# Kernel optimization log

Measured on AMD Instinct MI355X. Metric: run time of the kernel, lower is better.

The kernel has to match this reference:

```python
import jax, jax.numpy as jnp
import numpy as np

T_MIN, T_MAX = 0.6, 1.6
SIM_LO, SIM_HI = 0.5, 0.9
LN_EPS = 1e-5


def _layernorm(x, gamma, beta):
    mu = jnp.mean(x, axis=-1, keepdims=True)
    var = jnp.mean((x - mu) ** 2, axis=-1, keepdims=True)
    return (x - mu) * jax.lax.rsqrt(var + LN_EPS) * gamma + beta


def _cos_sim(a, b, eps=1e-8):
    num = jnp.sum(a * b, axis=-1)
    na = jnp.maximum(jnp.sqrt(jnp.sum(a * a, axis=-1)), eps)
    nb = jnp.maximum(jnp.sqrt(jnp.sum(b * b, axis=-1)), eps)
    return num / (na * nb)


def setup_inputs() -> dict:
    key = jax.random.key(0)
    B, L, D = 2, 4096, 512
    ks = jax.random.split(key, 10)
    s = 0.02
    return {
        "x": jax.random.normal(ks[0], (B, L, D), dtype=jnp.float32),
        "Wq": jax.random.normal(ks[1], (D, D), dtype=jnp.float32) * s,
        "Wk": jax.random.normal(ks[2], (D, D), dtype=jnp.float32) * s,
        "Wv": jax.random.normal(ks[3], (D, D), dtype=jnp.float32) * s,
        "Wp": jax.random.normal(ks[4], (D, D), dtype=jnp.float32) * s,
        "W1": jax.random.normal(ks[5], (4 * D, D), dtype=jnp.float32) * s,
        "b1": jnp.zeros((4 * D,), dtype=jnp.float32),
        "W2": jax.random.normal(ks[6], (D, 4 * D), dtype=jnp.float32) * s,
        "b2": jnp.zeros((D,), dtype=jnp.float32),
        "gamma": jnp.ones((D,), dtype=jnp.float32),
        "beta": jnp.zeros((D,), dtype=jnp.float32),
    }


def reference(x, Wq, Wk, Wv, Wp, W1, b1, W2, b2, gamma, beta):
    B, L, D = x.shape
    xn = _layernorm(x, gamma, beta)
    # TinyAttn with T=1.0, causal=True (torch Linear: x @ W.T)
    Q = jnp.einsum("bld,ed->ble", xn, Wq)
    K = jnp.einsum("bld,ed->ble", xn, Wk)
    V = jnp.einsum("bld,ed->ble", xn, Wv)
    scores = jnp.einsum("bld,bmd->blm", Q, K) / jnp.sqrt(jnp.asarray(D, x.dtype))
    causal = jnp.triu(jnp.ones((L, L), dtype=bool), 1)
    scores = jnp.where(causal, jnp.asarray(-1e30, x.dtype), scores)
    attn = jax.nn.softmax(scores, axis=-1)  # [B, L, L]
    out = jnp.einsum("blm,bmd->bld", attn, V)
    out = jnp.einsum("bld,ed->ble", out, Wp)
    ctx = x + out
    h = _layernorm(ctx, gamma, beta)
    h = jax.nn.gelu(jnp.einsum("bld,fd->blf", h, W1) + b1, approximate=False)
    ctx = ctx + jnp.einsum("blf,df->bld", h, W2) + b2

    # AdaptiveController on last-token attention row
    last_attn = attn[:, -1]  # [B, L]
    p = jnp.clip(last_attn, 1e-9, None)
    H = -jnp.sum(p * jnp.log(p), axis=-1)  # [B]
    Hn = (H - H.min()) / (H.max() - H.min() + 1e-9)
    Hm = jax.lax.stop_gradient(jnp.mean(Hn))  # detached in torch
    T = T_MIN + (T_MAX - T_MIN) * Hm
    sim_th = SIM_HI - (SIM_HI - SIM_LO) * Hm

    # UnconsciousStack: single forward -> stack holds only the just-pushed (K, V), detached.
    q_vec = jnp.mean(Q[:, -1], axis=0, keepdims=True)  # [1, D]
    K_rep = jax.lax.stop_gradient(jnp.mean(K, axis=1))  # [B, D]
    s = jnp.mean(_cos_sim(q_vec, K_rep))  # scalar
    hit = s >= sim_th

    K_cat = jnp.concatenate([K, jax.lax.stop_gradient(K)], axis=1)  # [B, 2L, D]
    V_cat = jnp.concatenate([V, jax.lax.stop_gradient(V)], axis=1)
    scores2 = jnp.einsum("bld,bmd->blm", Q, K_cat) / jnp.sqrt(jnp.asarray(D, x.dtype))
    attn2 = jax.nn.softmax(scores2 / T, axis=-1)  # [B, L, 2L], no causal mask
    reatt = jnp.einsum("blm,bmd->bld", attn2, V_cat)
    ctx = ctx + jnp.where(hit, reatt, jnp.zeros_like(reatt))
    return ctx
```

## Files before the change

### kernel.cpp

```cpp
#include <hip/hip_runtime.h>
#include <math.h>

#define BATCH 2
#define SEQ 4096
#define DIM 512
#define FF 2048
#define NROWS (BATCH*SEQ)
#define KT 32
#define RSQRT_D 0.044194173824159216f

typedef __attribute__((ext_vector_type(8))) short short8;
typedef __attribute__((ext_vector_type(4))) short short4v;
typedef __attribute__((ext_vector_type(4))) float f32x4;

__device__ __forceinline__ float gelu_f(float v) {
    return 0.5f * v * (1.0f + erff(v * 0.70710678118654752440f));
}
__device__ __forceinline__ short bf16b(float x) {
    union { float f; unsigned u; } c; c.f = x;
    unsigned r = (c.u + 0x7FFFu + ((c.u >> 16) & 1u)) >> 16;
    return (short)r;
}
__device__ __forceinline__ float bf16f(short h) {
    union { unsigned u; float f; } c; c.u = ((unsigned)(unsigned short)h) << 16;
    return c.f;
}
__device__ __forceinline__ void gload16(const void* g, void* l) {
    __builtin_amdgcn_global_load_lds(
        (const __attribute__((address_space(1))) unsigned int*)g,
        (__attribute__((address_space(3))) unsigned int*)l, 16, 0, 0);
}
__device__ __forceinline__ float blk_sum256(float v, volatile float* sm) {
    #pragma unroll
    for (int o = 32; o; o >>= 1) v += __shfl_xor(v, o);
    __syncthreads();
    if ((threadIdx.x & 63) == 0) sm[threadIdx.x >> 6] = v;
    __syncthreads();
    return sm[0] + sm[1] + sm[2] + sm[3];
}

__global__ __launch_bounds__(256) void f2bf_all(
        const float* __restrict__ Wq, const float* __restrict__ Wk,
        const float* __restrict__ Wv, const float* __restrict__ Wp,
        const float* __restrict__ W1, const float* __restrict__ W2,
        short* __restrict__ Wcat, short* __restrict__ Wpb,
        short* __restrict__ W1b, short* __restrict__ W2b)
{
    int i = blockIdx.x * 256 + threadIdx.x;
    const float* src; short* dst; int loc;
    if      (i <  32768) { src = Wq; dst = Wcat;          loc = i; }
    else if (i <  65536) { src = Wk; dst = Wcat + 262144; loc = i - 32768; }
    else if (i <  98304) { src = Wv; dst = Wcat + 524288; loc = i - 65536; }
    else if (i < 131072) { src = Wp; dst = Wpb;           loc = i - 98304; }
    else if (i < 262144) { src = W1; dst = W1b;           loc = i - 131072; }
    else                 { src = W2; dst = W2b;           loc = i - 262144; }
    const float4* p = (const float4*)(src + (size_t)loc * 8);
    float4 a = p[0], b = p[1];
    short8 r;
    r[0]=bf16b(a.x); r[1]=bf16b(a.y); r[2]=bf16b(a.z); r[3]=bf16b(a.w);
    r[4]=bf16b(b.x); r[5]=bf16b(b.y); r[6]=bf16b(b.z); r[7]=bf16b(b.w);
    *(short8*)(dst + (size_t)loc * 8) = r;
}

__global__ __launch_bounds__(256) void ln_kernel(const float* __restrict__ x,
        const float* __restrict__ g, const float* __restrict__ be,
        short* __restrict__ o)
{
    int row  = blockIdx.x * 4 + (threadIdx.x >> 6);
    int lane = threadIdx.x & 63;
    const float4* xr = (const float4*)(x + (size_t)row * DIM);
    float4 v0 = xr[lane*2], v1 = xr[lane*2+1];
    float s = v0.x+v0.y+v0.z+v0.w + v1.x+v1.y+v1.z+v1.w;
    #pragma unroll
    for (int off = 32; off; off >>= 1) s += __shfl_xor(s, off);
    float mu = s * (1.0f/DIM);
    float d[8] = {v0.x-mu, v0.y-mu, v0.z-mu, v0.w-mu, v1.x-mu, v1.y-mu, v1.z-mu, v1.w-mu};
    float q = 0.f;
    #pragma unroll
    for (int j = 0; j < 8; ++j) q += d[j]*d[j];
    #pragma unroll
    for (int off = 32; off; off >>= 1) q += __shfl_xor(q, off);
    float rs = rsqrtf(q * (1.0f/DIM) + 1e-5f);
    const float4* g4 = (const float4*)g;
    const float4* b4 = (const float4*)be;
    float4 ga = g4[lane*2], gb = g4[lane*2+1];
    float4 ba = b4[lane*2], bb = b4[lane*2+1];
    float gv[8] = {ga.x,ga.y,ga.z,ga.w, gb.x,gb.y,gb.z,gb.w};
    float bv[8] = {ba.x,ba.y,ba.z,ba.w, bb.x,bb.y,bb.z,bb.w};
    short8 r;
    #pragma unroll
    for (int j = 0; j < 8; ++j) r[j] = bf16b(d[j]*rs*gv[j] + bv[j]);
    *(short8*)(o + (size_t)row * DIM + lane*8) = r;
}

template<int TM, int TAG>
__global__ __launch_bounds__(256) void gemm_v4(
        const short* __restrict__ A, const short* __restrict__ W,
        const float* __restrict__ bias, const float* __restrict__ res,
        float* __restrict__ Cf, short* __restrict__ Cb,
        short* __restrict__ CbK, short* __restrict__ CbV,
        int K, int sa, int sw, int sc, int act, int accum)
{
    constexpr int MI = TM / 32;
    constexpr int ASZ = TM * 32;
    __shared__ short As[3 * ASZ];
    __shared__ short Ws[3 * 4096];
    int tid = threadIdx.x;
    int m0 = blockIdx.y * TM, n0 = blockIdx.x * 128;
    int w = tid >> 6, lane = tid & 63;
    int wr = (w >> 1) * (TM/2), wc = (w & 1) * 64;
    int lr = lane & 15, lg = lane >> 4;
    int srow = tid >> 2, skoff = (tid & 3) * 8;
    const short* Ab = A + (size_t)(m0 + srow) * sa + skoff;
    const short* Wb = W + (size_t)(n0 + srow) * sw + skoff;

    #define STAGE_G(buf, kk) do { \
        gload16(Ab + (kk),                    As + (buf)*ASZ + tid*8); \
        if constexpr (TM == 128) \
            gload16(Ab + (size_t)64*sa + (kk), As + (buf)*ASZ + 2048 + tid*8); \
        gload16(Wb + (kk),                    Ws + (buf)*4096 + tid*8); \
        gload16(Wb + (size_t)64*sw + (kk),    Ws + (buf)*4096 + 2048 + tid*8); } while(0)

    f32x4 acc[MI][4];
    f32x4 zero = {0.f, 0.f, 0.f, 0.f};
    #pragma unroll
    for (int i = 0; i < MI; ++i)
        #pragma unroll
        for (int j = 0; j < 4; ++j) acc[i][j] = zero;

    int NKB = K >> 5;
    STAGE_G(0, 0);
    STAGE_G(1, 32);
    int cur = 0;
    for (int kb = 0; kb < NKB; ++kb) {
        __builtin_amdgcn_s_barrier();
        asm volatile("" ::: "memory");
        if (kb + 2 < NKB) {
            int nb = cur + 2; if (nb >= 3) nb -= 3;
            STAGE_G(nb, (kb + 2) * 32);
            if constexpr (TM == 128) asm volatile("s_waitcnt vmcnt(8)" ::: "memory");
            else                     asm volatile("s_waitcnt vmcnt(6)" ::: "memory");
        } else if (kb + 1 < NKB) {
            if constexpr (TM == 128) asm volatile("s_waitcnt vmcnt(4)" ::: "memory");
            else                     asm volatile("s_waitcnt vmcnt(3)" ::: "memory");
        } else {
            asm volatile("s_waitcnt vmcnt(0)" ::: "memory");
        }
        __builtin_amdgcn_s_barrier();
        asm volatile("" ::: "memory");
        short8 a[MI], b[4];
        #pragma unroll
        for (int i = 0; i < MI; ++i) a[i] = *(const short8*)(As + cur*ASZ + (wr + i*16 + lr)*32 + lg*8);
        #pragma unroll
        for (int j = 0; j < 4; ++j) b[j] = *(const short8*)(Ws + cur*4096 + (wc + j*16 + lr)*32 + lg*8);
        #pragma unroll
        for (int i = 0; i < MI; ++i)
            #pragma unroll
            for (int j = 0; j < 4; ++j)
                acc[i][j] = __builtin_amdgcn_mfma_f32_16x16x32_bf16(a[i], b[j], acc[i][j], 0, 0, 0);
        cur = (cur + 1 == 3) ? 0 : cur + 1;
    }
    #undef STAGE_G

    #pragma unroll
    for (int i = 0; i < MI; ++i) {
        #pragma unroll
        for (int r = 0; r < 4; ++r) {
            size_t m = (size_t)m0 + wr + i*16 + lg*4 + r;
            #pragma unroll
            for (int j = 0; j < 4; ++j) {
                int n = n0 + wc + j*16 + lr;
                float v = acc[i][j][r];
                if (bias) v += bias[n];
                if (act)  v = gelu_f(v);
                if (CbK) {
                    int seg = n >> 9, nl = n & 511;
                    short* dst = (seg == 0) ? Cb : (seg == 1) ? CbK : CbV;
                    dst[m * 512 + nl] = bf16b(v);
                } else {
                    if (res) v += res[m * sc + n];
                    size_t idx = m * sc + n;
                    if (Cf) { if (accum) Cf[idx] += v; else Cf[idx] = v; }
                    if (Cb) Cb[idx] = bf16b(v);
                }
            }
        }
    }
}

__global__ __launch_bounds__(256) void vtrans(const short* __restrict__ V,
                                              short* __restrict__ Vt)
{
    __shared__ short t_s[64][72];
    int l0 = blockIdx.x * 64, d0 = blockIdx.y * 64, b = blockIdx.z;
    int t = threadIdx.x;
    const short* src = V + (size_t)b * SEQ * DIM;
    #pragma unroll
    for (int it = 0; it < 2; ++it) {
        int r = (t >> 3) + it * 32, c = (t & 7) * 8;
        *(short8*)&t_s[r][c] = *(const short8*)(src + (size_t)(l0 + r) * DIM + d0 + c);
    }
    __syncthreads();
    short* dst = Vt + (size_t)b * DIM * SEQ;
    #pragma unroll
    for (int it = 0; it < 2; ++it) {
        int r = (t >> 3) + it * 32, c = (t & 7) * 8;
        short8 v;
        #pragma unroll
        for (int j = 0; j < 8; ++j) v[j] = t_s[c + j][r];
        *(short8*)(dst + (size_t)(d0 + r) * SEQ + l0 + c) = v;
    }
}

__global__ __launch_bounds__(512, 2) void attn_v8(
        const short* __restrict__ Q, const short* __restrict__ K,
        const short* __restrict__ Vt, short* __restrict__ Opart,
        float* __restrict__ Mpart, float* __restrict__ Lpart,
        float scale, const float* __restrict__ scale_ptr,
        const float* __restrict__ gate, int causal, int NC, int ncs)
{
    if (gate && gate[0] == 0.0f) return;
    if (scale_ptr) scale = scale_ptr[0];
    extern __shared__ short lds[];
    short* k_s  = lds;
    short* v_s  = lds + 32768;
    short* p_s  = lds + 65536;
    float* ss_s = (float*)(lds + 69632);

    int tid = threadIdx.x, w = tid >> 6, lane = tid & 63;
    int rg = w >> 1, dh = w & 1;
    int lr = lane & 15, lg = lane >> 4;

    int bid = blockIdx.x;
    int c  = bid & (NC - 1);
    int b  = (bid >> ncs) & 1;
    int ip = bid >> (ncs + 1);
    int jj0 = ip, jj1 = 63 - ip;
    int TA = causal ? 2*(ip+1)  : 128;
    int TB = causal ? 2*(64-ip) : 128;
    int Ttot = TA + TB;
    int s0 = (Ttot * c) >> ncs, s1 = (Ttot * (c+1)) >> ncs;

    size_t bofs = (size_t)b * SEQ * DIM;
    size_t vofs = (size_t)b * DIM * SEQ;
    f32x4 zero = {0.f, 0.f, 0.f, 0.f};

    for (int sg = 0; sg < 2; ++sg) {
        int j  = sg ? jj1 : jj0;
        int ta = sg ? (max(s0, TA) - TA) : s0;
        int tb = sg ? (s1 - TA)          : min(s1, TA);
        if (ta >= tb) continue;
        int qw0 = j*64 + rg*16;

        short8 qf[8];
        #pragma unroll
        for (int kc = 0; kc < 8; ++kc)
            qf[kc] = *(const short8*)(Q + bofs + (size_t)(qw0 + lr)*DIM
                                      + dh*256 + kc*32 + lg*8);

        f32x4 o[16];
        #pragma unroll
        for (int df = 0; df < 16; ++df) o[df] = zero;
        float mreg[4] = {-1e30f,-1e30f,-1e30f,-1e30f};
        float lreg[4] = {0.f,0.f,0.f,0.f};
        int rowg[4];
        #pragma unroll
        for (int r = 0; r < 4; ++r) rowg[r] = qw0 + lg*4 + r;

        int cur = 0;
        {
            int k0s = ta * KT;
            #pragma unroll
            for (int s4 = 0; s4 < 4; ++s4) {
                int slot = tid + s4*512;
                int row = slot >> 6, cg = slot & 63;
                gload16(K + bofs + (size_t)(k0s + row)*DIM + ((cg ^ (row & 7)) << 3),
                        k_s + slot*8);
                int dpair = slot >> 3, low = slot & 7;
                int d = dpair*2 + (low & 1);
                int kg = (low >> 1) ^ (dpair & 3);
                gload16(Vt + vofs + (size_t)d*SEQ + k0s + kg*8,
                        v_s + slot*8);
            }
        }
        __syncthreads();

        for (int t = ta; t < tb; ++t) {
            int k0 = t * KT;
            if (t + 1 < tb) {
                int k0s = (t + 1) * KT;
                int bo = (cur ^ 1) * 16384;
                #pragma unroll
                for (int s4 = 0; s4 < 4; ++s4) {
                    int slot = tid + s4*512;
                    int row = slot >> 6, cg = slot & 63;
                    gload16(K + bofs + (size_t)(k0s + row)*DIM + ((cg ^ (row & 7)) << 3),
                            k_s + bo + slot*8);
                    int dpair = slot >> 3, low = slot & 7;
                    int d = dpair*2 + (low & 1);
                    int kg = (low >> 1) ^ (dpair & 3);
                    gload16(Vt + vofs + (size_t)d*SEQ + k0s + kg*8,
                            v_s + bo + slot*8);
                }
            }
            f32x4 ss[2];
            ss[0] = zero; ss[1] = zero;
            const short* kb = k_s + cur*16384;
            #pragma unroll
            for (int kc = 0; kc < 8; ++kc) {
                #pragma unroll
                for (int kf = 0; kf < 2; ++kf) {
                    int row = kf*16 + lr;
                    int dg = dh*32 + kc*4 + lg;
                    short8 kk = *(const short8*)(kb + row*512 + ((dg ^ (row & 7)) << 3));
                    ss[kf] = __builtin_amdgcn_mfma_f32_16x16x32_bf16(qf[kc], kk, ss[kf], 0, 0, 0);
                }
            }
            *(f32x4*)(ss_s + w*512 + lane*8)     = ss[0];
            *(f32x4*)(ss_s + w*512 + lane*8 + 4) = ss[1];
            asm volatile("s_waitcnt lgkmcnt(0)" ::: "memory");
            __builtin_amdgcn_s_barrier();
            __builtin_amdgcn_sched_barrier(0);
            f32x4 po0 = *(const f32x4*)(ss_s + (w^1)*512 + lane*8);
            f32x4 po1 = *(const f32x4*)(ss_s + (w^1)*512 + lane*8 + 4);
            bool needmask = causal && (k0 + KT - 1 > qw0);
            #pragma unroll
            for (int r = 0; r < 4; ++r) {
                float s0v = (ss[0][r] + po0[r]) * scale;
                float s1v = (ss[1][r] + po1[r]) * scale;
                if (needmask) {
                    if (k0 + lr      > rowg[r]) s0v = -1e30f;
                    if (k0 + 16 + lr > rowg[r]) s1v = -1e30f;
                }
                ss[0][r] = s0v; ss[1][r] = s1v;
            }
            float pm[4];
            bool tg = false;
            #pragma unroll
            for (int r = 0; r < 4; ++r) {
                pm[r] = fmaxf(ss[0][r], ss[1][r]);
                tg |= (pm[r] > mreg[r] + 8.0f);
            }
            if (__any(tg)) {
                #pragma unroll
                for (int r = 0; r < 4; ++r) {
                    float v = pm[r];
                    v = fmaxf(v, __shfl_xor(v, 1));
                    v = fmaxf(v, __shfl_xor(v, 2));
                    v = fmaxf(v, __shfl_xor(v, 4));
                    v = fmaxf(v, __shfl_xor(v, 8));
                    float nm = fmaxf(mreg[r], v);
                    float fr = __expf(mreg[r] - nm);
                    mreg[r] = nm;
                    lreg[r] *= fr;
                    #pragma unroll
                    for (int df = 0; df < 16; ++df) o[df][r] *= fr;
                }
            }
            #pragma unroll
            for (int kf = 0; kf < 2; ++kf) {
                #pragma unroll
                for (int r = 0; r < 4; ++r) {
                    float sv = ss[kf][r];
                    float p = (sv < -1e29f) ? 0.0f : __expf(sv - mreg[r]);
                    lreg[r] += p;
                    int row = lg*4 + r;
                    int oct = kf*2 + (lr >> 3);
                    p_s[w*512 + row*32 + ((oct ^ r ^ (lg & 3)) << 3) + (lr & 7)] = bf16b(p);
                }
            }
            short8 pa = *(const short8*)(p_s + w*512 + lr*32
                         + ((lg ^ (lr & 3) ^ ((lr >> 2) & 3)) << 3));
            const short* vb = v_s + cur*16384;
            #pragma unroll
            for (int df = 0; df < 16; ++df) {
                int d = dh*256 + df*16 + lr;
                int slot16 = (d >> 1)*8 + (((lg ^ ((d >> 1) & 3)) << 1) | (d & 1));
                short8 vv = *(const short8*)(vb + slot16*8);
                o[df] = __builtin_amdgcn_mfma_f32_16x16x32_bf16(pa, vv, o[df], 0, 0, 0);
            }
            __syncthreads();
            cur ^= 1;
        }

        #pragma unroll
        for (int r = 0; r < 4; ++r) {
            float v = lreg[r];
            v += __shfl_xor(v, 1);
            v += __shfl_xor(v, 2);
            v += __shfl_xor(v, 4);
            v += __shfl_xor(v, 8);
            lreg[r] = v;
        }
        int slot = (b*64 + j)*NC + c;
        size_t obase = ((size_t)slot*8 + w) * 4096;
        #pragma unroll
        for (int df = 0; df < 16; ++df) {
            short4v pk;
            #pragma unroll
            for (int r = 0; r < 4; ++r) pk[r] = bf16b(o[df][r]);
            *(short4v*)(Opart + obase + df*256 + lane*4) = pk;
        }
        if (dh == 0 && lr == 0) {
            #pragma unroll
            for (int r = 0; r < 4; ++r) {
                Mpart[slot*64 + rg*16 + lg*4 + r] = mreg[r];
                Lpart[slot*64 + rg*16 + lg*4 + r] = lreg[r];
            }
        }
    }
}

__global__ __launch_bounds__(256) void attn_merge(
        const short* __restrict__ Opart, const float* __restrict__ Mpart,
        const float* __restrict__ Lpart, short* __restrict__ attb,
        float* __restrict__ outf, const float* __restrict__ gate,
        int causal, int NC, int ncs)
{
    if (gate && gate[0] == 0.0f) return;
    __shared__ float wts[8][64];
    int j = blockIdx.x, dh = blockIdx.y, b = blockIdx.z;
    int tid = threadIdx.x;
    int ip = (j < 32) ? j : 63 - j;
    int TA = causal ? 2*(ip+1)  : 128;
    int TB = causal ? 2*(64-ip) : 128;
    int Ttot = TA + TB;
    int jstart = (j < 32) ? 0 : TA;
    int jend   = (j < 32) ? TA : Ttot;
    bool val[8];
    for (int c = 0; c < 8; ++c) {
        int sc = (Ttot * c) >> ncs, ec = (Ttot * (c+1)) >> ncs;
        val[c] = (c < NC) && (sc < jend) && (ec > jstart);
    }
    if (tid < 64) {
        float M = -1e30f;
        for (int c = 0; c < NC; ++c)
            if (val[c]) M = fmaxf(M, Mpart[((b*64 + j)*NC + c)*64 + tid]);
        float L = 0.f;
        for (int c = 0; c < NC; ++c)
            if (val[c]) L += Lpart[((b*64 + j)*NC + c)*64 + tid]
                           * __expf(Mpart[((b*64 + j)*NC + c)*64 + tid] - M);
        float invL = 1.0f / L;
        for (int c = 0; c < NC; ++c)
            wts[c][tid] = val[c]
                ? __expf(Mpart[((b*64 + j)*NC + c)*64 + tid] - M) * invL : 0.0f;
    }
    __syncthreads();
    int wv = tid >> 6, lane = tid & 63, lg = lane >> 4, lr = lane & 15;
    int region = wv*2 + dh;
    for (int df = 0; df < 16; ++df) {
        float acc[4] = {0.f, 0.f, 0.f, 0.f};
        for (int c = 0; c < NC; ++c) {
            if (!val[c]) continue;
            size_t idx = ((size_t)((b*64 + j)*NC + c)*8 + region)*4096 + df*256 + lane*4;
            short4v v = *(const short4v*)(Opart + idx);
            #pragma unroll
            for (int r = 0; r < 4; ++r)
                acc[r] += wts[c][wv*16 + lg*4 + r] * bf16f(v[r]);
        }
        #pragma unroll
        for (int r = 0; r < 4; ++r) {
            int row = j*64 + wv*16 + lg*4 + r;
            int d = dh*256 + df*16 + lr;
            size_t oidx = (size_t)b*SEQ*DIM + (size_t)row*DIM + d;
            if (attb) attb[oidx] = bf16b(acc[r]);
            else      outf[oidx] += acc[r];
        }
    }
}

__global__ __launch_bounds__(256) void lastrow_scores(const short* __restrict__ Q,
        const short* __restrict__ K, float* __restrict__ slast)
{
    __shared__ float q_l[DIM];
    int b = blockIdx.y;
    int m = blockIdx.x * 256 + threadIdx.x;
    for (int i = threadIdx.x; i < DIM; i += 256)
        q_l[i] = bf16f(Q[((size_t)b*SEQ + SEQ-1)*DIM + i]);
    __syncthreads();
    const short* kr = K + ((size_t)b*SEQ + m) * DIM;
    float s = 0.f;
    for (int d = 0; d < DIM; d += 8) {
        short8 k8 = *(const short8*)(kr + d);
        #pragma unroll
        for (int j = 0; j < 8; ++j) s += q_l[d + j] * bf16f(k8[j]);
    }
    slast[(size_t)b*SEQ + m] = s * RSQRT_D;
}

__global__ __launch_bounds__(256) void entropy_kernel(const float* __restrict__ slast,
        float* __restrict__ H)
{
    __shared__ float sm[4];
    int b = blockIdx.x, t = threadIdx.x;
    const float* s = slast + (size_t)b * SEQ;
    float v[16];
    float mx = -1e30f;
    #pragma unroll
    for (int j = 0; j < 16; ++j) { v[j] = s[t + j*256]; mx = fmaxf(mx, v[j]); }
    #pragma unroll
    for (int o = 32; o; o >>= 1) mx = fmaxf(mx, __shfl_xor(mx, o));
    __syncthreads();
    if ((t & 63) == 0) sm[t >> 6] = mx;
    __syncthreads();
    mx = fmaxf(fmaxf(sm[0], sm[1]), fmaxf(sm[2], sm[3]));
    float se = 0.f;
    #pragma unroll
    for (int j = 0; j < 16; ++j) { v[j] = expf(v[j] - mx); se += v[j]; }
    se = blk_sum256(se, sm);
    float inv = 1.0f / se;
    float h = 0.f;
    #pragma unroll
    for (int j = 0; j < 16; ++j) {
        float p = fmaxf(v[j] * inv, 1e-9f);
        h -= p * logf(p);
    }
    h = blk_sum256(h, sm);
    if (t == 0) H[b] = h;
}

__global__ __launch_bounds__(256) void krep_partial(const short* __restrict__ K,
        float* __restrict__ part)
{
    int b = blockIdx.y, j = blockIdx.x, t = threadIdx.x;
    size_t base = ((size_t)b*SEQ + (size_t)j*64) * DIM;
    float s0 = 0.f, s1 = 0.f;
    for (int r = 0; r < 64; ++r) {
        s0 += bf16f(K[base + (size_t)r*DIM + t]);
        s1 += bf16f(K[base + (size_t)r*DIM + t + 256]);
    }
    size_t o = (size_t)(b*64 + j) * DIM;
    part[o + t] = s0; part[o + t + 256] = s1;
}

__global__ __launch_bounds__(256) void scalar_kernel(const short* __restrict__ Qb,
        const float* __restrict__ part, const float* __restrict__ Hent,
        float* __restrict__ gsc)
{
    __shared__ float sm[4];
    __shared__ float sims[BATCH];
    int t = threadIdx.x;
    float qv0 = 0.5f*(bf16f(Qb[((size_t)0*SEQ + SEQ-1)*DIM + t])     + bf16f(Qb[((size_t)1*SEQ + SEQ-1)*DIM + t]));
    float qv1 = 0.5f*(bf16f(Qb[((size_t)0*SEQ + SEQ-1)*DIM + t+256]) + bf16f(Qb[((size_t)1*SEQ + SEQ-1)*DIM + t+256]));
    for (int b = 0; b < BATCH; ++b) {
        float k0 = 0.f, k1 = 0.f;
        for (int j = 0; j < 64; ++j) {
            k0 += part[(size_t)(b*64+j)*DIM + t];
            k1 += part[(size_t)(b*64+j)*DIM + t + 256];
        }
        k0 *= (1.0f/SEQ); k1 *= (1.0f/SEQ);
        float num = blk_sum256(qv0*k0 + qv1*k1, sm);
        float qq  = blk_sum256(qv0*qv0 + qv1*qv1, sm);
        float kk  = blk_sum256(k0*k0 + k1*k1, sm);
        if (t == 0) {
            float na = fmaxf(sqrtf(qq), 1e-8f);
            float nb = fmaxf(sqrtf(kk), 1e-8f);
            sims[b] = num / (na * nb);
        }
        __syncthreads();
    }
    if (t == 0) {
        float H0 = Hent[0], H1 = Hent[1];
        float mn = fminf(H0, H1), mx = fmaxf(H0, H1);
        float den = (mx - mn) + 1e-9f;
        float Hm = 0.5f*((H0 - mn)/den + (H1 - mn)/den);
        float T  = 0.6f + (1.6f - 0.6f) * Hm;
        float th = 0.9f - (0.9f - 0.5f) * Hm;
        float s  = 0.5f * (sims[0] + sims[1]);
        gsc[0] = (s >= th) ? 1.0f : 0.0f;
        gsc[1] = 1.0f / (sqrtf((float)DIM) * T);
    }
}

extern "C" void kernel_launch(void* const* d_in, const int* in_sizes, int n_in,
                              void* d_out, int out_size, void* d_ws, size_t ws_size,
                              hipStream_t stream)
{
    (void)in_sizes; (void)n_in; (void)out_size;
    const float* x     = (const float*)d_in[0];
    const float* Wq    = (const float*)d_in[1];
    const float* Wk    = (const float*)d_in[2];
    const float* Wv    = (const float*)d_in[3];
    const float* Wp    = (const float*)d_in[4];
    const float* W1    = (const float*)d_in[5];
    const float* b1    = (const float*)d_in[6];
    const float* W2    = (const float*)d_in[7];
    const float* b2    = (const float*)d_in[8];
    const float* gamma = (const float*)d_in[9];
    const float* beta  = (const float*)d_in[10];
    float* out = (float*)d_out;

    const size_t NT = (size_t)NROWS * DIM;
    short* bws   = (short*)d_ws;
    short* Qbf   = bws;
    short* Kbf   = Qbf + NT;
    short* Vt    = Kbf + NT;
    short* att   = Vt + NT;
    short* Wcat  = att + NT;
    short* Wpb   = Wcat + 786432;
    short* W1b   = Wpb + 262144;
    short* W2b   = W1b + 1048576;
    float* slast = (float*)(W2b + 1048576);
    float* Hent  = slast + 8192;
    float* kpart = Hent + 8;
    float* gsc   = kpart + 65536;

    const int NC = 4, ncs = 2;
    size_t mlsz = (size_t)128 * NC * 64;
    float* Mpart = gsc + 8;
    float* Lpart = Mpart + mlsz;
    short* xn_bf = (short*)(Lpart + mlsz);
    short* h1    = xn_bf + NT;
    short* Opart = xn_bf;

    size_t ffn_full_end = ((size_t)(h1 - bws) + (size_t)NROWS * FF) * 2;
    int ffn_full = (ws_size >= ffn_full_end + 1024);

    const int ATTN_LDS = 155648;
    hipFuncSetAttribute((const void*)attn_v8,
                        hipFuncAttributeMaxDynamicSharedMemorySize, ATTN_LDS);

    f2bf_all<<<1536, 256, 0, stream>>>(Wq, Wk, Wv, Wp, W1, W2, Wcat, Wpb, W1b, W2b);

    ln_kernel<<<NROWS/4, 256, 0, stream>>>(x, gamma, beta, xn_bf);

    gemm_v4<128,0><<<dim3(1536/128, NROWS/128), 256, 0, stream>>>(
        xn_bf, Wcat, nullptr, nullptr, nullptr, Qbf, Kbf, att,
        DIM, DIM, DIM, DIM, 0, 0);
    vtrans<<<dim3(SEQ/64, DIM/64, BATCH), 256, 0, stream>>>(att, Vt);

    attn_v8<<<64*NC, 512, ATTN_LDS, stream>>>(Qbf, Kbf, Vt, Opart, Mpart, Lpart,
                                              RSQRT_D, nullptr, nullptr, 1, NC, ncs);
    attn_merge<<<dim3(64, 2, BATCH), 256, 0, stream>>>(Opart, Mpart, Lpart, att, nullptr,
                                                       nullptr, 1, NC, ncs);

    lastrow_scores<<<dim3(SEQ/256, BATCH), 256, 0, stream>>>(Qbf, Kbf, slast);
    entropy_kernel<<<BATCH, 256, 0, stream>>>(slast, Hent);

    gemm_v4<64,1><<<dim3(DIM/128, NROWS/64), 256, 0, stream>>>(
        att, Wpb, nullptr, x, out, nullptr, nullptr, nullptr,
        DIM, DIM, DIM, DIM, 0, 0);

    ln_kernel<<<NROWS/4, 256, 0, stream>>>(out, gamma, beta, xn_bf);

    if (ffn_full) {
        gemm_v4<128,2><<<dim3(FF/128, NROWS/128), 256, 0, stream>>>(
            xn_bf, W1b, b1, nullptr, nullptr, h1, nullptr, nullptr,
            DIM, DIM, DIM, FF, 1, 0);
        gemm_v4<64,3><<<dim3(DIM/128, NROWS/64), 256, 0, stream>>>(
            h1, W2b, b2, nullptr, out, nullptr, nullptr, nullptr,
            FF, FF, FF, DIM, 0, 1);
    } else {
        for (int c = 0; c < 2; ++c) {
            gemm_v4<128,2><<<dim3(1024/128, NROWS/128), 256, 0, stream>>>(
                xn_bf, W1b + (size_t)c*1024*DIM, b1 + c*1024, nullptr,
                nullptr, h1, nullptr, nullptr,
                DIM, DIM, DIM, 1024, 1, 0);
            gemm_v4<64,3><<<dim3(DIM/128, NROWS/64), 256, 0, stream>>>(
                h1, W2b + (size_t)c*1024, (c == 0) ? b2 : nullptr, nullptr,
                out, nullptr, nullptr, nullptr,
                1024, 1024, FF, DIM, 0, 1);
        }
    }

    krep_partial<<<dim3(64, BATCH), 256, 0, stream>>>(Kbf, kpart);
    scalar_kernel<<<1, 256, 0, stream>>>(Qbf, kpart, Hent, gsc);

    attn_v8<<<64*NC, 512, ATTN_LDS, stream>>>(Qbf, Kbf, Vt, Opart, Mpart, Lpart,
                                              0.0f, gsc + 1, gsc, 0, NC, ncs);
    attn_merge<<<dim3(64, 2, BATCH), 256, 0, stream>>>(Opart, Mpart, Lpart, nullptr, out,
                                                       gsc, 0, NC, ncs);
}
```

Baseline: 337.3 us.

## Double key tile to 64, single-buffer K/V with split prefetch, bf16 score exchange

The attention kernel now processes 64 keys per iteration instead of 32. It drops the K/V double buffer in favour of a single buffer, where the next K tile is loaded after the score barrier and the next V tile after the PV stage. The partial QK scores exchanged between the two d-halves go through LDS as bf16 instead of fp32, reusing one scratch area that also holds P. This aims to halve the number of iterations and barriers per tile and to raise MFMA work per sync, at the cost of less load/compute overlap and lower precision in the summed scores.

```diff
diff --git a/kernel.cpp b/kernel.cpp
--- a/kernel.cpp
+++ b/kernel.cpp
@@ -6,7 +6,7 @@
 #define DIM 512
 #define FF 2048
 #define NROWS (BATCH*SEQ)
-#define KT 32
+#define KTL 64
 #define RSQRT_D 0.044194173824159216f
 
 typedef __attribute__((ext_vector_type(8))) short short8;
@@ -212,7 +212,7 @@
     }
 }
 
-__global__ __launch_bounds__(512, 2) void attn_v8(
+__global__ __launch_bounds__(512, 2) void attn_v9(
         const short* __restrict__ Q, const short* __restrict__ K,
         const short* __restrict__ Vt, short* __restrict__ Opart,
         float* __restrict__ Mpart, float* __restrict__ Lpart,
@@ -222,10 +222,9 @@
     if (gate && gate[0] == 0.0f) return;
     if (scale_ptr) scale = scale_ptr[0];
     extern __shared__ short lds[];
-    short* k_s  = lds;
-    short* v_s  = lds + 32768;
-    short* p_s  = lds + 65536;
-    float* ss_s = (float*)(lds + 69632);
+    short* k_s = lds;
+    short* v_s = lds + 32768;
+    short* ex  = lds + 65536;
 
     int tid = threadIdx.x, w = tid >> 6, lane = tid & 63;
     int rg = w >> 1, dh = w & 1;
@@ -235,9 +234,8 @@
     int c  = bid & (NC - 1);
     int b  = (bid >> ncs) & 1;
     int ip = bid >> (ncs + 1);
-    int jj0 = ip, jj1 = 63 - ip;
-    int TA = causal ? 2*(ip+1)  : 128;
-    int TB = causal ? 2*(64-ip) : 128;
+    int TA = causal ? (ip + 1)  : 64;
+    int TB = causal ? (64 - ip) : 64;
     int Ttot = TA + TB;
     int s0 = (Ttot * c) >> ncs, s1 = (Ttot * (c+1)) >> ncs;
 
@@ -246,7 +244,7 @@
     f32x4 zero = {0.f, 0.f, 0.f, 0.f};
 
     for (int sg = 0; sg < 2; ++sg) {
-        int j  = sg ? jj1 : jj0;
+        int j  = sg ? (63 - ip) : ip;
         int ta = sg ? (max(s0, TA) - TA) : s0;
         int tb = sg ? (s1 - TA)          : min(s1, TA);
         if (ta >= tb) continue;
@@ -267,78 +265,83 @@
         #pragma unroll
         for (int r = 0; r < 4; ++r) rowg[r] = qw0 + lg*4 + r;
 
-        int cur = 0;
         {
-            int k0s = ta * KT;
-            #pragma unroll
-            for (int s4 = 0; s4 < 4; ++s4) {
-                int slot = tid + s4*512;
+            int k0s = ta * KTL;
+            #pragma unroll
+            for (int i = 0; i < 8; ++i) {
+                int slot = tid + i*512;
                 int row = slot >> 6, cg = slot & 63;
                 gload16(K + bofs + (size_t)(k0s + row)*DIM + ((cg ^ (row & 7)) << 3),
                         k_s + slot*8);
-                int dpair = slot >> 3, low = slot & 7;
-                int d = dpair*2 + (low & 1);
-                int kg = (low >> 1) ^ (dpair & 3);
-                gload16(Vt + vofs + (size_t)d*SEQ + k0s + kg*8,
+                int d = slot >> 3, od = slot & 7;
+                gload16(Vt + vofs + (size_t)d*SEQ + k0s + ((od ^ (d & 7)) << 3),
                         v_s + slot*8);
             }
         }
         __syncthreads();
 
         for (int t = ta; t < tb; ++t) {
-            int k0 = t * KT;
-            if (t + 1 < tb) {
-                int k0s = (t + 1) * KT;
-                int bo = (cur ^ 1) * 16384;
+            int k0 = t * KTL;
+            bool pre = (t + 1 < tb);
+            f32x4 ss[4];
+            #pragma unroll
+            for (int kf = 0; kf < 4; ++kf) ss[kf] = zero;
+            #pragma unroll
+            for (int kc = 0; kc < 8; ++kc) {
+                int dg = dh*32 + kc*4 + lg;
                 #pragma unroll
-                for (int s4 = 0; s4 < 4; ++s4) {
-                    int slot = tid + s4*512;
+                for (int kf = 0; kf < 4; ++kf) {
+                    int row = kf*16 + lr;
+                    short8 kk = *(const short8*)(k_s + row*512 + ((dg ^ (row & 7)) << 3));
+                    ss[kf] = __builtin_amdgcn_mfma_f32_16x16x32_bf16(qf[kc], kk, ss[kf], 0, 0, 0);
+                }
+            }
+            short8 pk0, pk1;
+            #pragma unroll
+            for (int r = 0; r < 4; ++r) {
+                pk0[r]   = bf16b(ss[0][r]); pk0[4+r] = bf16b(ss[1][r]);
+                pk1[r]   = bf16b(ss[2][r]); pk1[4+r] = bf16b(ss[3][r]);
+            }
+            *(short8*)(ex + w*1024 + lane*16)     = pk0;
+            *(short8*)(ex + w*1024 + lane*16 + 8) = pk1;
+            __syncthreads();
+            if (pre) {
+                int k0s = (t + 1) * KTL;
+                #pragma unroll
+                for (int i = 0; i < 8; ++i) {
+                    int slot = tid + i*512;
                     int row = slot >> 6, cg = slot & 63;
                     gload16(K + bofs + (size_t)(k0s + row)*DIM + ((cg ^ (row & 7)) << 3),
-                            k_s + bo + slot*8);
-                    int dpair = slot >> 3, low = slot & 7;
-                    int d = dpair*2 + (low & 1);
-                    int kg = (low >> 1) ^ (dpair & 3);
-                    gload16(Vt + vofs + (size_t)d*SEQ + k0s + kg*8,
-                            v_s + bo + slot*8);
-                }
-            }
-            f32x4 ss[2];
-            ss[0] = zero; ss[1] = zero;
-            const short* kb = k_s + cur*16384;
-            #pragma unroll
-            for (int kc = 0; kc < 8; ++kc) {
-                #pragma unroll
-                for (int kf = 0; kf < 2; ++kf) {
-                    int row = kf*16 + lr;
-                    int dg = dh*32 + kc*4 + lg;
-                    short8 kk = *(const short8*)(kb + row*512 + ((dg ^ (row & 7)) << 3));
-                    ss[kf] = __builtin_amdgcn_mfma_f32_16x16x32_bf16(qf[kc], kk, ss[kf], 0, 0, 0);
-                }
-            }
-            *(f32x4*)(ss_s + w*512 + lane*8)     = ss[0];
-            *(f32x4*)(ss_s + w*512 + lane*8 + 4) = ss[1];
+                            k_s + slot*8);
+                }
+            }
+            short8 po0 = *(const short8*)(ex + (w^1)*1024 + lane*16);
+            short8 po1 = *(const short8*)(ex + (w^1)*1024 + lane*16 + 8);
             asm volatile("s_waitcnt lgkmcnt(0)" ::: "memory");
             __builtin_amdgcn_s_barrier();
             __builtin_amdgcn_sched_barrier(0);
-            f32x4 po0 = *(const f32x4*)(ss_s + (w^1)*512 + lane*8);
-            f32x4 po1 = *(const f32x4*)(ss_s + (w^1)*512 + lane*8 + 4);
-            bool needmask = causal && (k0 + KT - 1 > qw0);
+            bool needmask = causal && (k0 + KTL - 1 > qw0);
             #pragma unroll
             for (int r = 0; r < 4; ++r) {
-                float s0v = (ss[0][r] + po0[r]) * scale;
-                float s1v = (ss[1][r] + po1[r]) * scale;
-                if (needmask) {
-                    if (k0 + lr      > rowg[r]) s0v = -1e30f;
-                    if (k0 + 16 + lr > rowg[r]) s1v = -1e30f;
-                }
-                ss[0][r] = s0v; ss[1][r] = s1v;
+                ss[0][r] = (bf16f(pk0[r])   + bf16f(po0[r]))   * scale;
+                ss[1][r] = (bf16f(pk0[4+r]) + bf16f(po0[4+r])) * scale;
+                ss[2][r] = (bf16f(pk1[r])   + bf16f(po1[r]))   * scale;
+                ss[3][r] = (bf16f(pk1[4+r]) + bf16f(po1[4+r])) * scale;
+            }
+            if (needmask) {
+                #pragma unroll
+                for (int kf = 0; kf < 4; ++kf) {
+                    int key = k0 + kf*16 + lr;
+                    #pragma unroll
+                    for (int r = 0; r < 4; ++r)
+                        if (key > rowg[r]) ss[kf][r] = -1e30f;
+                }
             }
             float pm[4];
             bool tg = false;
             #pragma unroll
             for (int r = 0; r < 4; ++r) {
-                pm[r] = fmaxf(ss[0][r], ss[1][r]);
+                pm[r] = fmaxf(fmaxf(ss[0][r], ss[1][r]), fmaxf(ss[2][r], ss[3][r]));
                 tg |= (pm[r] > mreg[r] + 8.0f);
             }
             if (__any(tg)) {
@@ -358,29 +361,42 @@
                 }
             }
             #pragma unroll
-            for (int kf = 0; kf < 2; ++kf) {
+            for (int kf = 0; kf < 4; ++kf) {
+                int oct = kf*2 + (lr >> 3);
                 #pragma unroll
                 for (int r = 0; r < 4; ++r) {
                     float sv = ss[kf][r];
                     float p = (sv < -1e29f) ? 0.0f : __expf(sv - mreg[r]);
                     lreg[r] += p;
                     int row = lg*4 + r;
-                    int oct = kf*2 + (lr >> 3);
-                    p_s[w*512 + row*32 + ((oct ^ r ^ (lg & 3)) << 3) + (lr & 7)] = bf16b(p);
-                }
-            }
-            short8 pa = *(const short8*)(p_s + w*512 + lr*32
-                         + ((lg ^ (lr & 3) ^ ((lr >> 2) & 3)) << 3));
-            const short* vb = v_s + cur*16384;
+                    ex[w*1024 + row*64 + ((oct ^ (row & 7)) << 3) + (lr & 7)] = bf16b(p);
+                }
+            }
+            short8 pa[2];
+            #pragma unroll
+            for (int ks = 0; ks < 2; ++ks)
+                pa[ks] = *(const short8*)(ex + w*1024 + lr*64
+                          + (((ks*4 + lg) ^ (lr & 7)) << 3));
             #pragma unroll
             for (int df = 0; df < 16; ++df) {
                 int d = dh*256 + df*16 + lr;
-                int slot16 = (d >> 1)*8 + (((lg ^ ((d >> 1) & 3)) << 1) | (d & 1));
-                short8 vv = *(const short8*)(vb + slot16*8);
-                o[df] = __builtin_amdgcn_mfma_f32_16x16x32_bf16(pa, vv, o[df], 0, 0, 0);
+                #pragma unroll
+                for (int ks = 0; ks < 2; ++ks) {
+                    short8 vv = *(const short8*)(v_s + d*64 + (((ks*4 + lg) ^ (d & 7)) << 3));
+                    o[df] = __builtin_amdgcn_mfma_f32_16x16x32_bf16(pa[ks], vv, o[df], 0, 0, 0);
+                }
             }
             __syncthreads();
-            cur ^= 1;
+            if (pre) {
+                int k0s = (t + 1) * KTL;
+                #pragma unroll
+                for (int i = 0; i < 8; ++i) {
+                    int slot = tid + i*512;
+                    int d = slot >> 3, od = slot & 7;
+                    gload16(Vt + vofs + (size_t)d*SEQ + k0s + ((od ^ (d & 7)) << 3),
+                            v_s + slot*8);
+                }
+            }
         }
 
         #pragma unroll
@@ -422,8 +438,8 @@
     int j = blockIdx.x, dh = blockIdx.y, b = blockIdx.z;
     int tid = threadIdx.x;
     int ip = (j < 32) ? j : 63 - j;
-    int TA = causal ? 2*(ip+1)  : 128;
-    int TB = causal ? 2*(64-ip) : 128;
+    int TA = causal ? (ip + 1)  : 64;
+    int TB = causal ? (64 - ip) : 64;
     int Ttot = TA + TB;
     int jstart = (j < 32) ? 0 : TA;
     int jend   = (j < 32) ? TA : Ttot;
@@ -616,8 +632,8 @@
     size_t ffn_full_end = ((size_t)(h1 - bws) + (size_t)NROWS * FF) * 2;
     int ffn_full = (ws_size >= ffn_full_end + 1024);
 
-    const int ATTN_LDS = 155648;
-    hipFuncSetAttribute((const void*)attn_v8,
+    const int ATTN_LDS = 147456;
+    hipFuncSetAttribute((const void*)attn_v9,
                         hipFuncAttributeMaxDynamicSharedMemorySize, ATTN_LDS);
 
     f2bf_all<<<1536, 256, 0, stream>>>(Wq, Wk, Wv, Wp, W1, W2, Wcat, Wpb, W1b, W2b);
@@ -629,7 +645,7 @@
         DIM, DIM, DIM, DIM, 0, 0);
     vtrans<<<dim3(SEQ/64, DIM/64, BATCH), 256, 0, stream>>>(att, Vt);
 
-    attn_v8<<<64*NC, 512, ATTN_LDS, stream>>>(Qbf, Kbf, Vt, Opart, Mpart, Lpart,
+    attn_v9<<<64*NC, 512, ATTN_LDS, stream>>>(Qbf, Kbf, Vt, Opart, Mpart, Lpart,
                                               RSQRT_D, nullptr, nullptr, 1, NC, ncs);
     attn_merge<<<dim3(64, 2, BATCH), 256, 0, stream>>>(Opart, Mpart, Lpart, att, nullptr,
                                                        nullptr, 1, NC, ncs);
@@ -666,7 +682,7 @@
     krep_partial<<<dim3(64, BATCH), 256, 0, stream>>>(Kbf, kpart);
     scalar_kernel<<<1, 256, 0, stream>>>(Qbf, kpart, Hent, gsc);
 
-    attn_v8<<<64*NC, 512, ATTN_LDS, stream>>>(Qbf, Kbf, Vt, Opart, Mpart, Lpart,
+    attn_v9<<<64*NC, 512, ATTN_LDS, stream>>>(Qbf, Kbf, Vt, Opart, Mpart, Lpart,
                                               0.0f, gsc + 1, gsc, 0, NC, ncs);
     attn_merge<<<dim3(64, 2, BATCH), 256, 0, stream>>>(Opart, Mpart, Lpart, nullptr, out,
                                                        gsc, 0, NC, ncs);
```

Result: no change. 339.3 us (+0.6%).
